# Performance work log

Measured on AMD Instinct MI355X. Metric: run time of the kernel, lower is better.

The kernel has to match this reference:

```python
import jax, jax.numpy as jnp
import numpy as np

N, E = 50000, 640000
D_IN, D_OUT, N_BASES = 128, 128, 8


def setup_inputs() -> dict:
    key = jax.random.key(0)
    k1, k2, k3, k4, k5, k6 = jax.random.split(key, 6)
    x = jax.random.normal(k1, (N, D_IN), dtype=jnp.float32)
    edge_index = jax.random.randint(k2, (2, E), 0, N, dtype=jnp.int64)
    # basis-decomposed relation weights (num_relations=1)
    bases = jax.random.normal(k3, (N_BASES, D_IN, D_OUT), dtype=jnp.float32) * 0.05
    comp = jax.random.normal(k4, (1, N_BASES), dtype=jnp.float32)
    root = jax.random.normal(k5, (D_IN, D_OUT), dtype=jnp.float32) * 0.05
    bias = jax.random.normal(k6, (D_OUT,), dtype=jnp.float32) * 0.01
    return {"x": x, "edge_index": edge_index, "bases": bases,
            "comp": comp, "root": root, "bias": bias}


def reference(x, edge_index, bases, comp, root, bias):
    # W[rel=0] = sum_b comp[0,b] * bases[b]  -> [D_IN, D_OUT]
    W = jnp.einsum('b,bio->io', comp[0], bases)
    src = edge_index[0]  # message sources (x_j)
    dst = edge_index[1]  # aggregation targets
    # gather -> scatter-add (aggr='add'), then relation-specific transform
    agg = jax.ops.segment_sum(x[src], dst, num_segments=x.shape[0])  # [N, D_IN]
    out = agg @ W + x @ root + bias  # root/self-loop transform + bias
    return out
```

## Files before the change

kernel.cpp:

```cpp
#include <hip/hip_runtime.h>

#define N_NODES 50000
#define N_EDGES 640000
#define D 128
#define NB 8
#define PAD 32
#define NSTRIP 3125

#define BUCKET_B 256
#define GEMM_B   768

typedef _Float16 half_t;
typedef __attribute__((ext_vector_type(8))) _Float16 half8;
typedef __attribute__((ext_vector_type(4))) float f32x4;

__global__ __launch_bounds__(256)
void init_kernel(const float* __restrict__ bases,
                 const float* __restrict__ comp,
                 const float* __restrict__ root,
                 half_t* __restrict__ Wt,
                 half_t* __restrict__ Rt,
                 int* __restrict__ cnt,
                 int* __restrict__ novf) {
    int i = blockIdx.x * 256 + threadIdx.x;
    if (i == 0) *novf = 0;
    if (i < N_NODES) cnt[i] = 0;
    if (i < D * D) {
        int ii = i >> 7, o = i & 127;
        float acc = 0.f;
#pragma unroll
        for (int b = 0; b < NB; ++b)
            acc += comp[b] * bases[((size_t)b * D + ii) * D + o];
        Wt[o * D + ii] = (half_t)acc;
        Rt[o * D + ii] = (half_t)root[i];
    }
}

__global__ __launch_bounds__(256, 4)
void fused_kernel(const float* __restrict__ x,
                  const half_t* __restrict__ Wt,
                  const half_t* __restrict__ Rt,
                  const float* __restrict__ bias,
                  const int* __restrict__ eidx,
                  half_t* __restrict__ y,
                  float* __restrict__ out,
                  int* __restrict__ cnt,
                  int* __restrict__ bucket,
                  int* __restrict__ ovf,
                  int* __restrict__ novf) {
    const int tid = threadIdx.x;

    if (blockIdx.x < BUCKET_B) {
        int t = blockIdx.x * 256 + tid;
        for (int e = t; e < N_EDGES; e += BUCKET_B * 256) {
            int src = eidx[e];
            int dst = eidx[N_EDGES + e];
            int pos = atomicAdd(&cnt[dst], 1);
            if (pos < PAD) {
                bucket[(size_t)dst * PAD + pos] = src;
            } else {
                int k = atomicAdd(novf, 1);
                ovf[2 * k]     = src;
                ovf[2 * k + 1] = dst;
            }
        }
        return;
    }

    const int gb   = blockIdx.x - BUCKET_B;
    const int wave = tid >> 6;
    const int lane = tid & 63;
    const int m    = lane & 15;
    const int quad = lane >> 4;
    const int q    = wave;
    const int s0   = gb;
    const int SSTR = GEMM_B;

    half8 bw[2][4], br[2][4];
    float bb[2];
#pragma unroll
    for (int t = 0; t < 2; ++t) {
        const int nt = 2 * q + t;
        const half_t* wp = Wt + (nt * 16 + m) * D + quad * 8;
        const half_t* rp = Rt + (nt * 16 + m) * D + quad * 8;
#pragma unroll
        for (int kk = 0; kk < 4; ++kk) {
            bw[t][kk] = *(const half8*)(wp + kk * 32);
            br[t][kk] = *(const half8*)(rp + kk * 32);
        }
        bb[t] = bias[nt * 16 + m];
    }

    const float4* x4 = (const float4*)x;
    for (int s = s0; s < NSTRIP; s += SSTR) {
        size_t ab = (size_t)(s * 16 + m) * 32 + quad * 2;
        half8 a[4];
#pragma unroll
        for (int kk = 0; kk < 4; ++kk) {
            float4 v0 = x4[ab + kk * 8];
            float4 v1 = x4[ab + kk * 8 + 1];
            half8 h;
            h[0] = (half_t)v0.x; h[1] = (half_t)v0.y; h[2] = (half_t)v0.z; h[3] = (half_t)v0.w;
            h[4] = (half_t)v1.x; h[5] = (half_t)v1.y; h[6] = (half_t)v1.z; h[7] = (half_t)v1.w;
            a[kk] = h;
        }

        f32x4 accW[2], accR[2];
#pragma unroll
        for (int t = 0; t < 2; ++t) {
            accW[t] = (f32x4){0.f, 0.f, 0.f, 0.f};
            accR[t] = (f32x4){0.f, 0.f, 0.f, 0.f};
        }
#pragma unroll
        for (int t = 0; t < 2; ++t)
#pragma unroll
            for (int kk = 0; kk < 4; ++kk) {
                accW[t] = __builtin_amdgcn_mfma_f32_16x16x32_f16(a[kk], bw[t][kk], accW[t], 0, 0, 0);
                accR[t] = __builtin_amdgcn_mfma_f32_16x16x32_f16(a[kk], br[t][kk], accR[t], 0, 0, 0);
            }

#pragma unroll
        for (int t = 0; t < 2; ++t) {
            int col = (2 * q + t) * 16 + m;
#pragma unroll
            for (int r = 0; r < 4; ++r) {
                int row = s * 16 + quad * 4 + r;
                y[(size_t)row * D + col]   = (half_t)accW[t][r];
                out[(size_t)row * D + col] = accR[t][r] + bb[t];
            }
        }
    }
}

__global__ __launch_bounds__(256)
void gather_kernel(const int* __restrict__ cnt,
                   const int* __restrict__ bucket,
                   const half_t* __restrict__ y,
                   const int* __restrict__ ovf,
                   const int* __restrict__ novf,
                   float* __restrict__ out) {
    int node = blockIdx.x * 16 + (threadIdx.x >> 4);
    int q = threadIdx.x & 15;
    if (node >= N_NODES) return;
    int c_raw = cnt[node];
    int c = c_raw > PAD ? PAD : c_raw;
    const int* b = bucket + (size_t)node * PAD;
    float acc[8] = {0.f, 0.f, 0.f, 0.f, 0.f, 0.f, 0.f, 0.f};
    int i = 0;
    for (; i + 8 <= c; i += 8) {
        int4 s0 = *(const int4*)(b + i);
        int4 s1 = *(const int4*)(b + i + 4);
        half8 v0 = *(const half8*)(y + (size_t)s0.x * D + q * 8);
        half8 v1 = *(const half8*)(y + (size_t)s0.y * D + q * 8);
        half8 v2 = *(const half8*)(y + (size_t)s0.z * D + q * 8);
        half8 v3 = *(const half8*)(y + (size_t)s0.w * D + q * 8);
        half8 v4 = *(const half8*)(y + (size_t)s1.x * D + q * 8);
        half8 v5 = *(const half8*)(y + (size_t)s1.y * D + q * 8);
        half8 v6 = *(const half8*)(y + (size_t)s1.z * D + q * 8);
        half8 v7 = *(const half8*)(y + (size_t)s1.w * D + q * 8);
#pragma unroll
        for (int j = 0; j < 8; ++j)
            acc[j] += ((float)v0[j] + (float)v1[j]) + ((float)v2[j] + (float)v3[j])
                    + ((float)v4[j] + (float)v5[j]) + ((float)v6[j] + (float)v7[j]);
    }
    for (; i + 4 <= c; i += 4) {
        int4 s = *(const int4*)(b + i);
        half8 v0 = *(const half8*)(y + (size_t)s.x * D + q * 8);
        half8 v1 = *(const half8*)(y + (size_t)s.y * D + q * 8);
        half8 v2 = *(const half8*)(y + (size_t)s.z * D + q * 8);
        half8 v3 = *(const half8*)(y + (size_t)s.w * D + q * 8);
#pragma unroll
        for (int j = 0; j < 8; ++j)
            acc[j] += ((float)v0[j] + (float)v1[j]) + ((float)v2[j] + (float)v3[j]);
    }
    for (; i < c; ++i) {
        half8 v = *(const half8*)(y + (size_t)b[i] * D + q * 8);
#pragma unroll
        for (int j = 0; j < 8; ++j) acc[j] += (float)v[j];
    }
    if (c_raw > PAD) {
        int n = *novf;
        for (int k = 0; k < n; ++k) {
            if (ovf[2 * k + 1] == node) {
                half8 v = *(const half8*)(y + (size_t)ovf[2 * k] * D + q * 8);
#pragma unroll
                for (int j = 0; j < 8; ++j) acc[j] += (float)v[j];
            }
        }
    }
    float4* op = (float4*)(out + (size_t)node * D + q * 8);
    float4 o0 = op[0], o1 = op[1];
    o0.x += acc[0]; o0.y += acc[1]; o0.z += acc[2]; o0.w += acc[3];
    o1.x += acc[4]; o1.y += acc[5]; o1.z += acc[6]; o1.w += acc[7];
    op[0] = o0; op[1] = o1;
}

extern "C" void kernel_launch(void* const* d_in, const int* in_sizes, int n_in,
                              void* d_out, int out_size, void* d_ws, size_t ws_size,
                              hipStream_t stream) {
    const float* x     = (const float*)d_in[0];
    const int*   eidx  = (const int*)d_in[1];
    const float* bases = (const float*)d_in[2];
    const float* comp  = (const float*)d_in[3];
    const float* root  = (const float*)d_in[4];
    const float* bias  = (const float*)d_in[5];
    float* out = (float*)d_out;

    char* ws = (char*)d_ws;
    half_t* y      = (half_t*)ws;
    half_t* Wt     = (half_t*)(ws + 12800000);
    half_t* Rt     = (half_t*)(ws + 12832768);
    int*    cnt    = (int*)   (ws + 12865536);
    int*    bucket = (int*)   (ws + 13065536);
    int*    novf   = (int*)   (ws + 19465536);
    int*    ovf    = (int*)   (ws + 19465552);

    init_kernel<<<(N_NODES + 255) / 256, 256, 0, stream>>>(
        bases, comp, root, Wt, Rt, cnt, novf);
    fused_kernel<<<BUCKET_B + GEMM_B, 256, 0, stream>>>(
        x, Wt, Rt, bias, eidx, y, out, cnt, bucket, ovf, novf);
    gather_kernel<<<(N_NODES + 15) / 16, 256, 0, stream>>>(
        cnt, bucket, y, ovf, novf, out);
}
```

Measured before the change: 148.1 us.

## Aggregate fp16 x before transform and fuse gather with GEMM epilogue

The order of operations changes from transform-then-gather to gather-then-transform. Stage 1 buckets edges and converts x to fp16, and stage 2 gathers neighbour rows of xh into LDS per 16-node tile. It then runs the W and root MFMAs and writes out once. This removes the fp32 out read-modify-write and the separate y write, but rounds the aggregated sum to fp16 before the GEMM and reloads weights from global memory per block.

```diff
diff --git a/kernel.cpp b/kernel.cpp
--- a/kernel.cpp
+++ b/kernel.cpp
@@ -5,10 +5,10 @@
 #define D 128
 #define NB 8
 #define PAD 32
-#define NSTRIP 3125
-
-#define BUCKET_B 256
-#define GEMM_B   768
+#define NBLK2 3125
+
+#define K1_GRID   2048
+#define K1_BUCKET 1024
 
 typedef _Float16 half_t;
 typedef __attribute__((ext_vector_type(8))) _Float16 half8;
@@ -36,23 +36,18 @@
     }
 }
 
-__global__ __launch_bounds__(256, 4)
-void fused_kernel(const float* __restrict__ x,
-                  const half_t* __restrict__ Wt,
-                  const half_t* __restrict__ Rt,
-                  const float* __restrict__ bias,
-                  const int* __restrict__ eidx,
-                  half_t* __restrict__ y,
-                  float* __restrict__ out,
-                  int* __restrict__ cnt,
-                  int* __restrict__ bucket,
-                  int* __restrict__ ovf,
-                  int* __restrict__ novf) {
+__global__ __launch_bounds__(256)
+void stage1_kernel(const float* __restrict__ x,
+                   const int* __restrict__ eidx,
+                   half_t* __restrict__ xh,
+                   int* __restrict__ cnt,
+                   int* __restrict__ bucket,
+                   int* __restrict__ ovf,
+                   int* __restrict__ novf) {
     const int tid = threadIdx.x;
-
-    if (blockIdx.x < BUCKET_B) {
+    if (blockIdx.x < K1_BUCKET) {
         int t = blockIdx.x * 256 + tid;
-        for (int e = t; e < N_EDGES; e += BUCKET_B * 256) {
+        for (int e = t; e < N_EDGES; e += K1_BUCKET * 256) {
             int src = eidx[e];
             int dst = eidx[N_EDGES + e];
             int pos = atomicAdd(&cnt[dst], 1);
@@ -66,43 +61,104 @@
         }
         return;
     }
-
-    const int gb   = blockIdx.x - BUCKET_B;
-    const int wave = tid >> 6;
-    const int lane = tid & 63;
-    const int m    = lane & 15;
-    const int quad = lane >> 4;
-    const int q    = wave;
-    const int s0   = gb;
-    const int SSTR = GEMM_B;
-
-    half8 bw[2][4], br[2][4];
-    float bb[2];
-#pragma unroll
-    for (int t = 0; t < 2; ++t) {
-        const int nt = 2 * q + t;
-        const half_t* wp = Wt + (nt * 16 + m) * D + quad * 8;
-        const half_t* rp = Rt + (nt * 16 + m) * D + quad * 8;
+    const int UNITS = N_NODES * D / 8;
+    const int STR   = (K1_GRID - K1_BUCKET) * 256;
+    const float4* x4 = (const float4*)x;
+    for (int u = (blockIdx.x - K1_BUCKET) * 256 + tid; u < UNITS; u += STR) {
+        float4 v0 = x4[2 * (size_t)u];
+        float4 v1 = x4[2 * (size_t)u + 1];
+        half8 h;
+        h[0] = (half_t)v0.x; h[1] = (half_t)v0.y; h[2] = (half_t)v0.z; h[3] = (half_t)v0.w;
+        h[4] = (half_t)v1.x; h[5] = (half_t)v1.y; h[6] = (half_t)v1.z; h[7] = (half_t)v1.w;
+        *(half8*)(xh + (size_t)u * 8) = h;
+    }
+}
+
+__global__ __launch_bounds__(256)
+void stage2_kernel(const half_t* __restrict__ xh,
+                   const half_t* __restrict__ Wt,
+                   const half_t* __restrict__ Rt,
+                   const float* __restrict__ bias,
+                   const int* __restrict__ cnt,
+                   const int* __restrict__ bucket,
+                   const int* __restrict__ ovf,
+                   const int* __restrict__ novf,
+                   float* __restrict__ out) {
+    __shared__ half_t ldsA[16 * 136];
+    __shared__ float  ldsO[16 * 132];
+
+    const int tid = threadIdx.x;
+    const int nb  = blockIdx.x;
+
+    {
+        int nrow = tid >> 4;
+        int q    = tid & 15;
+        int node = nb * 16 + nrow;
+        int c_raw = cnt[node];
+        int c = c_raw > PAD ? PAD : c_raw;
+        const int* b = bucket + (size_t)node * PAD;
+        float acc[8] = {0.f, 0.f, 0.f, 0.f, 0.f, 0.f, 0.f, 0.f};
+        int i = 0;
+        for (; i + 8 <= c; i += 8) {
+            int4 s0 = *(const int4*)(b + i);
+            int4 s1 = *(const int4*)(b + i + 4);
+            half8 v0 = *(const half8*)(xh + (size_t)s0.x * D + q * 8);
+            half8 v1 = *(const half8*)(xh + (size_t)s0.y * D + q * 8);
+            half8 v2 = *(const half8*)(xh + (size_t)s0.z * D + q * 8);
+            half8 v3 = *(const half8*)(xh + (size_t)s0.w * D + q * 8);
+            half8 v4 = *(const half8*)(xh + (size_t)s1.x * D + q * 8);
+            half8 v5 = *(const half8*)(xh + (size_t)s1.y * D + q * 8);
+            half8 v6 = *(const half8*)(xh + (size_t)s1.z * D + q * 8);
+            half8 v7 = *(const half8*)(xh + (size_t)s1.w * D + q * 8);
+#pragma unroll
+            for (int j = 0; j < 8; ++j)
+                acc[j] += ((float)v0[j] + (float)v1[j]) + ((float)v2[j] + (float)v3[j])
+                        + ((float)v4[j] + (float)v5[j]) + ((float)v6[j] + (float)v7[j]);
+        }
+        for (; i + 4 <= c; i += 4) {
+            int4 s = *(const int4*)(b + i);
+            half8 v0 = *(const half8*)(xh + (size_t)s.x * D + q * 8);
+            half8 v1 = *(const half8*)(xh + (size_t)s.y * D + q * 8);
+            half8 v2 = *(const half8*)(xh + (size_t)s.z * D + q * 8);
+            half8 v3 = *(const half8*)(xh + (size_t)s.w * D + q * 8);
+#pragma unroll
+            for (int j = 0; j < 8; ++j)
+                acc[j] += ((float)v0[j] + (float)v1[j]) + ((float)v2[j] + (float)v3[j]);
+        }
+        for (; i < c; ++i) {
+            half8 v = *(const half8*)(xh + (size_t)b[i] * D + q * 8);
+#pragma unroll
+            for (int j = 0; j < 8; ++j) acc[j] += (float)v[j];
+        }
+        if (c_raw > PAD) {
+            int n = *novf;
+            for (int k = 0; k < n; ++k) {
+                if (ovf[2 * k + 1] == node) {
+                    half8 v = *(const half8*)(xh + (size_t)ovf[2 * k] * D + q * 8);
+#pragma unroll
+                    for (int j = 0; j < 8; ++j) acc[j] += (float)v[j];
+                }
+            }
+        }
+        half8 h;
+#pragma unroll
+        for (int j = 0; j < 8; ++j) h[j] = (half_t)acc[j];
+        *(half8*)(ldsA + nrow * 136 + q * 8) = h;
+    }
+    __syncthreads();
+
+    {
+        const int wave = tid >> 6;
+        const int lane = tid & 63;
+        const int m    = lane & 15;
+        const int quad = lane >> 4;
+
+        half8 a[4], a2[4];
+        const half_t* xrow = xh + (size_t)(nb * 16 + m) * D;
 #pragma unroll
         for (int kk = 0; kk < 4; ++kk) {
-            bw[t][kk] = *(const half8*)(wp + kk * 32);
-            br[t][kk] = *(const half8*)(rp + kk * 32);
-        }
-        bb[t] = bias[nt * 16 + m];
-    }
-
-    const float4* x4 = (const float4*)x;
-    for (int s = s0; s < NSTRIP; s += SSTR) {
-        size_t ab = (size_t)(s * 16 + m) * 32 + quad * 2;
-        half8 a[4];
-#pragma unroll
-        for (int kk = 0; kk < 4; ++kk) {
-            float4 v0 = x4[ab + kk * 8];
-            float4 v1 = x4[ab + kk * 8 + 1];
-            half8 h;
-            h[0] = (half_t)v0.x; h[1] = (half_t)v0.y; h[2] = (half_t)v0.z; h[3] = (half_t)v0.w;
-            h[4] = (half_t)v1.x; h[5] = (half_t)v1.y; h[6] = (half_t)v1.z; h[7] = (half_t)v1.w;
-            a[kk] = h;
+            a[kk]  = *(const half8*)(ldsA + m * 136 + (4 * kk + quad) * 8);
+            a2[kk] = *(const half8*)(xrow + kk * 32 + quad * 8);
         }
 
         f32x4 accW[2], accR[2];
@@ -112,87 +168,39 @@
             accR[t] = (f32x4){0.f, 0.f, 0.f, 0.f};
         }
 #pragma unroll
-        for (int t = 0; t < 2; ++t)
+        for (int t = 0; t < 2; ++t) {
+            const int nt = 2 * wave + t;
+            const half_t* wp = Wt + (nt * 16 + m) * D + quad * 8;
+            const half_t* rp = Rt + (nt * 16 + m) * D + quad * 8;
 #pragma unroll
             for (int kk = 0; kk < 4; ++kk) {
-                accW[t] = __builtin_amdgcn_mfma_f32_16x16x32_f16(a[kk], bw[t][kk], accW[t], 0, 0, 0);
-                accR[t] = __builtin_amdgcn_mfma_f32_16x16x32_f16(a[kk], br[t][kk], accR[t], 0, 0, 0);
+                half8 bw = *(const half8*)(wp + kk * 32);
+                half8 br = *(const half8*)(rp + kk * 32);
+                accW[t] = __builtin_amdgcn_mfma_f32_16x16x32_f16(a[kk],  bw, accW[t], 0, 0, 0);
+                accR[t] = __builtin_amdgcn_mfma_f32_16x16x32_f16(a2[kk], br, accR[t], 0, 0, 0);
             }
+        }
 
 #pragma unroll
         for (int t = 0; t < 2; ++t) {
-            int col = (2 * q + t) * 16 + m;
-#pragma unroll
-            for (int r = 0; r < 4; ++r) {
-                int row = s * 16 + quad * 4 + r;
-                y[(size_t)row * D + col]   = (half_t)accW[t][r];
-                out[(size_t)row * D + col] = accR[t][r] + bb[t];
-            }
-        }
-    }
-}
-
-__global__ __launch_bounds__(256)
-void gather_kernel(const int* __restrict__ cnt,
-                   const int* __restrict__ bucket,
-                   const half_t* __restrict__ y,
-                   const int* __restrict__ ovf,
-                   const int* __restrict__ novf,
-                   float* __restrict__ out) {
-    int node = blockIdx.x * 16 + (threadIdx.x >> 4);
-    int q = threadIdx.x & 15;
-    if (node >= N_NODES) return;
-    int c_raw = cnt[node];
-    int c = c_raw > PAD ? PAD : c_raw;
-    const int* b = bucket + (size_t)node * PAD;
-    float acc[8] = {0.f, 0.f, 0.f, 0.f, 0.f, 0.f, 0.f, 0.f};
-    int i = 0;
-    for (; i + 8 <= c; i += 8) {
-        int4 s0 = *(const int4*)(b + i);
-        int4 s1 = *(const int4*)(b + i + 4);
-        half8 v0 = *(const half8*)(y + (size_t)s0.x * D + q * 8);
-        half8 v1 = *(const half8*)(y + (size_t)s0.y * D + q * 8);
-        half8 v2 = *(const half8*)(y + (size_t)s0.z * D + q * 8);
-        half8 v3 = *(const half8*)(y + (size_t)s0.w * D + q * 8);
-        half8 v4 = *(const half8*)(y + (size_t)s1.x * D + q * 8);
-        half8 v5 = *(const half8*)(y + (size_t)s1.y * D + q * 8);
-        half8 v6 = *(const half8*)(y + (size_t)s1.z * D + q * 8);
-        half8 v7 = *(const half8*)(y + (size_t)s1.w * D + q * 8);
-#pragma unroll
-        for (int j = 0; j < 8; ++j)
-            acc[j] += ((float)v0[j] + (float)v1[j]) + ((float)v2[j] + (float)v3[j])
-                    + ((float)v4[j] + (float)v5[j]) + ((float)v6[j] + (float)v7[j]);
-    }
-    for (; i + 4 <= c; i += 4) {
-        int4 s = *(const int4*)(b + i);
-        half8 v0 = *(const half8*)(y + (size_t)s.x * D + q * 8);
-        half8 v1 = *(const half8*)(y + (size_t)s.y * D + q * 8);
-        half8 v2 = *(const half8*)(y + (size_t)s.z * D + q * 8);
-        half8 v3 = *(const half8*)(y + (size_t)s.w * D + q * 8);
-#pragma unroll
-        for (int j = 0; j < 8; ++j)
-            acc[j] += ((float)v0[j] + (float)v1[j]) + ((float)v2[j] + (float)v3[j]);
-    }
-    for (; i < c; ++i) {
-        half8 v = *(const half8*)(y + (size_t)b[i] * D + q * 8);
-#pragma unroll
-        for (int j = 0; j < 8; ++j) acc[j] += (float)v[j];
-    }
-    if (c_raw > PAD) {
-        int n = *novf;
-        for (int k = 0; k < n; ++k) {
-            if (ovf[2 * k + 1] == node) {
-                half8 v = *(const half8*)(y + (size_t)ovf[2 * k] * D + q * 8);
-#pragma unroll
-                for (int j = 0; j < 8; ++j) acc[j] += (float)v[j];
-            }
-        }
-    }
-    float4* op = (float4*)(out + (size_t)node * D + q * 8);
-    float4 o0 = op[0], o1 = op[1];
-    o0.x += acc[0]; o0.y += acc[1]; o0.z += acc[2]; o0.w += acc[3];
-    o1.x += acc[4]; o1.y += acc[5]; o1.z += acc[6]; o1.w += acc[7];
-    op[0] = o0; op[1] = o1;
+            const int nt = 2 * wave + t;
+            float bb = bias[nt * 16 + m];
+#pragma unroll
+            for (int r = 0; r < 4; ++r)
+                ldsO[(quad * 4 + r) * 132 + nt * 16 + m] = accW[t][r] + accR[t][r] + bb;
+        }
+    }
+    __syncthreads();
+
+    {
+        int row = tid >> 4, cq = tid & 15;
+        const float* src = ldsO + row * 132 + cq * 8;
+        float4 o0 = *(const float4*)(src);
+        float4 o1 = *(const float4*)(src + 4);
+        float4* op = (float4*)(out + (size_t)(nb * 16 + row) * D + cq * 8);
+        op[0] = o0;
+        op[1] = o1;
+    }
 }
 
 extern "C" void kernel_launch(void* const* d_in, const int* in_sizes, int n_in,
@@ -207,7 +215,7 @@
     float* out = (float*)d_out;
 
     char* ws = (char*)d_ws;
-    half_t* y      = (half_t*)ws;
+    half_t* xh     = (half_t*)ws;
     half_t* Wt     = (half_t*)(ws + 12800000);
     half_t* Rt     = (half_t*)(ws + 12832768);
     int*    cnt    = (int*)   (ws + 12865536);
@@ -217,8 +225,8 @@
 
     init_kernel<<<(N_NODES + 255) / 256, 256, 0, stream>>>(
         bases, comp, root, Wt, Rt, cnt, novf);
-    fused_kernel<<<BUCKET_B + GEMM_B, 256, 0, stream>>>(
-        x, Wt, Rt, bias, eidx, y, out, cnt, bucket, ovf, novf);
-    gather_kernel<<<(N_NODES + 15) / 16, 256, 0, stream>>>(
-        cnt, bucket, y, ovf, novf, out);
-}
+    stage1_kernel<<<K1_GRID, 256, 0, stream>>>(
+        x, eidx, xh, cnt, bucket, ovf, novf);
+    stage2_kernel<<<NBLK2, 256, 0, stream>>>(
+        xh, Wt, Rt, bias, cnt, bucket, ovf, novf, out);
+}
```

After: 179.6 us. 1.21x slower.

## Split each node's neighbor gather across a full wave with padded zero-row loads

Applied to the files above, without the earlier changes.

The gather kernel now gives each node a full 64-lane wave instead of a 16-lane group. The four 16-lane sub-groups each take a quarter of the node's bucket and issue a fixed 8 independent row loads. Unused slots point at a new all-zero sentinel row appended to y, and the partial sums are combined with cross-lane shuffles. The goal is to expose more memory-level parallelism and remove the serial, data-dependent loop over neighbors. The cost is 4x more waves, redundant sentinel loads that mostly hit cache, and workspace offsets shifted to make room for the zero row.

```diff
diff --git a/kernel.cpp b/kernel.cpp
--- a/kernel.cpp
+++ b/kernel.cpp
@@ -20,11 +20,13 @@
                  const float* __restrict__ root,
                  half_t* __restrict__ Wt,
                  half_t* __restrict__ Rt,
+                 half_t* __restrict__ y,
                  int* __restrict__ cnt,
                  int* __restrict__ novf) {
     int i = blockIdx.x * 256 + threadIdx.x;
     if (i == 0) *novf = 0;
     if (i < N_NODES) cnt[i] = 0;
+    if (i < D) y[(size_t)N_NODES * D + i] = (half_t)0.f;
     if (i < D * D) {
         int ii = i >> 7, o = i & 127;
         float acc = 0.f;
@@ -139,60 +141,60 @@
                    const int* __restrict__ ovf,
                    const int* __restrict__ novf,
                    float* __restrict__ out) {
-    int node = blockIdx.x * 16 + (threadIdx.x >> 4);
-    int q = threadIdx.x & 15;
+    const int wave = threadIdx.x >> 6;
+    const int lane = threadIdx.x & 63;
+    const int g    = lane >> 4;
+    const int q    = lane & 15;
+    const int node = blockIdx.x * 4 + wave;
     if (node >= N_NODES) return;
+
     int c_raw = cnt[node];
     int c = c_raw > PAD ? PAD : c_raw;
-    const int* b = bucket + (size_t)node * PAD;
-    float acc[8] = {0.f, 0.f, 0.f, 0.f, 0.f, 0.f, 0.f, 0.f};
-    int i = 0;
-    for (; i + 8 <= c; i += 8) {
-        int4 s0 = *(const int4*)(b + i);
-        int4 s1 = *(const int4*)(b + i + 4);
-        half8 v0 = *(const half8*)(y + (size_t)s0.x * D + q * 8);
-        half8 v1 = *(const half8*)(y + (size_t)s0.y * D + q * 8);
-        half8 v2 = *(const half8*)(y + (size_t)s0.z * D + q * 8);
-        half8 v3 = *(const half8*)(y + (size_t)s0.w * D + q * 8);
-        half8 v4 = *(const half8*)(y + (size_t)s1.x * D + q * 8);
-        half8 v5 = *(const half8*)(y + (size_t)s1.y * D + q * 8);
-        half8 v6 = *(const half8*)(y + (size_t)s1.z * D + q * 8);
-        half8 v7 = *(const half8*)(y + (size_t)s1.w * D + q * 8);
-#pragma unroll
-        for (int j = 0; j < 8; ++j)
-            acc[j] += ((float)v0[j] + (float)v1[j]) + ((float)v2[j] + (float)v3[j])
-                    + ((float)v4[j] + (float)v5[j]) + ((float)v6[j] + (float)v7[j]);
-    }
-    for (; i + 4 <= c; i += 4) {
-        int4 s = *(const int4*)(b + i);
-        half8 v0 = *(const half8*)(y + (size_t)s.x * D + q * 8);
-        half8 v1 = *(const half8*)(y + (size_t)s.y * D + q * 8);
-        half8 v2 = *(const half8*)(y + (size_t)s.z * D + q * 8);
-        half8 v3 = *(const half8*)(y + (size_t)s.w * D + q * 8);
-#pragma unroll
-        for (int j = 0; j < 8; ++j)
-            acc[j] += ((float)v0[j] + (float)v1[j]) + ((float)v2[j] + (float)v3[j]);
-    }
-    for (; i < c; ++i) {
-        half8 v = *(const half8*)(y + (size_t)b[i] * D + q * 8);
-#pragma unroll
-        for (int j = 0; j < 8; ++j) acc[j] += (float)v[j];
-    }
+    const int* bp = bucket + (size_t)node * PAD;
+
+    int base = (c * g) >> 2;
+    int ng   = ((c * (g + 1)) >> 2) - base;
+
+    int idx[8];
+#pragma unroll
+    for (int j = 0; j < 8; ++j)
+        idx[j] = (j < ng) ? bp[base + j] : N_NODES;
+
+    half8 v[8];
+#pragma unroll
+    for (int j = 0; j < 8; ++j)
+        v[j] = *(const half8*)(y + (size_t)idx[j] * D + q * 8);
+
+    float acc[8];
+#pragma unroll
+    for (int t = 0; t < 8; ++t)
+        acc[t] = (((float)v[0][t] + (float)v[1][t]) + ((float)v[2][t] + (float)v[3][t]))
+               + (((float)v[4][t] + (float)v[5][t]) + ((float)v[6][t] + (float)v[7][t]));
+
     if (c_raw > PAD) {
         int n = *novf;
-        for (int k = 0; k < n; ++k) {
+        for (int k = g; k < n; k += 4) {
             if (ovf[2 * k + 1] == node) {
-                half8 v = *(const half8*)(y + (size_t)ovf[2 * k] * D + q * 8);
-#pragma unroll
-                for (int j = 0; j < 8; ++j) acc[j] += (float)v[j];
-            }
-        }
-    }
-    float4* op = (float4*)(out + (size_t)node * D + q * 8);
-    float4 o0 = op[0], o1 = op[1];
-    o0.x += acc[0]; o0.y += acc[1]; o0.z += acc[2]; o0.w += acc[3];
-    o1.x += acc[4]; o1.y += acc[5]; o1.z += acc[6]; o1.w += acc[7];
-    op[0] = o0; op[1] = o1;
+                half8 w = *(const half8*)(y + (size_t)ovf[2 * k] * D + q * 8);
+#pragma unroll
+                for (int t = 0; t < 8; ++t) acc[t] += (float)w[t];
+            }
+        }
+    }
+
+#pragma unroll
+    for (int t = 0; t < 8; ++t) {
+        acc[t] += __shfl_xor(acc[t], 16);
+        acc[t] += __shfl_xor(acc[t], 32);
+    }
+
+    if (g == 0) {
+        float4* op = (float4*)(out + (size_t)node * D + q * 8);
+        float4 o0 = op[0], o1 = op[1];
+        o0.x += acc[0]; o0.y += acc[1]; o0.z += acc[2]; o0.w += acc[3];
+        o1.x += acc[4]; o1.y += acc[5]; o1.z += acc[6]; o1.w += acc[7];
+        op[0] = o0; op[1] = o1;
+    }
 }
 
 extern "C" void kernel_launch(void* const* d_in, const int* in_sizes, int n_in,
@@ -208,17 +210,17 @@
 
     char* ws = (char*)d_ws;
     half_t* y      = (half_t*)ws;
-    half_t* Wt     = (half_t*)(ws + 12800000);
-    half_t* Rt     = (half_t*)(ws + 12832768);
-    int*    cnt    = (int*)   (ws + 12865536);
-    int*    bucket = (int*)   (ws + 13065536);
-    int*    novf   = (int*)   (ws + 19465536);
-    int*    ovf    = (int*)   (ws + 19465552);
+    half_t* Wt     = (half_t*)(ws + 12800512);
+    half_t* Rt     = (half_t*)(ws + 12833280);
+    int*    cnt    = (int*)   (ws + 12866048);
+    int*    bucket = (int*)   (ws + 13066048);
+    int*    novf   = (int*)   (ws + 19466048);
+    int*    ovf    = (int*)   (ws + 19466064);
 
     init_kernel<<<(N_NODES + 255) / 256, 256, 0, stream>>>(
-        bases, comp, root, Wt, Rt, cnt, novf);
+        bases, comp, root, Wt, Rt, y, cnt, novf);
     fused_kernel<<<BUCKET_B + GEMM_B, 256, 0, stream>>>(
         x, Wt, Rt, bias, eidx, y, out, cnt, bucket, ovf, novf);
-    gather_kernel<<<(N_NODES + 15) / 16, 256, 0, stream>>>(
+    gather_kernel<<<(N_NODES + 3) / 4, 256, 0, stream>>>(
         cnt, bucket, y, ovf, novf, out);
 }
```

New measurement: 153.1 us. 3.4% more time.
